# Optimization experiments

Hardware: AMD Instinct MI355X
Metric: run time of the kernel (lower is better)

Reference implementation:

```python
import jax, jax.numpy as jnp
import numpy as np

H = 128            # hidden_channels
HM = 2 * H         # _inner_mlp_mult * H
N = 50000          # num nodes
E = 400000         # num edges
M = 800000         # num node-edge incidences (2 per edge)
BN_EPS = 1e-5


def _bn_relu(x, g, b):
    # BatchNorm1d in training mode: population stats over the batch dim, then affine + ReLU
    m = x.mean(0)
    v = ((x - m) ** 2).mean(0)
    return jax.nn.relu((x - m) * jax.lax.rsqrt(v + BN_EPS) * g + b)


def setup_inputs() -> dict:
    key = jax.random.key(0)
    ks = jax.random.split(key, 12)
    node_rep = jax.random.normal(ks[0], (N, H), dtype=jnp.float32)
    edge_rep = jax.random.normal(ks[1], (E, H), dtype=jnp.float32)
    src = jax.random.randint(ks[2], (M,), 0, N, dtype=jnp.int32)
    dst = jax.random.randint(ks[3], (M,), 0, E, dtype=jnp.int32)
    node2edge_index = jnp.stack([src, dst], 0)

    def lin(k, fan_in, fan_out):
        return jax.random.normal(k, (fan_in, fan_out), dtype=jnp.float32) / np.sqrt(fan_in)

    return {
        "node_rep": node_rep,
        "edge_rep": edge_rep,
        "node2edge_index": node2edge_index,
        # lvl_mlp_1: Linear(2H->H, no bias), BN(H), ReLU
        "Wa": lin(ks[4], 2 * H, H), "ga": jnp.ones((H,)), "ba": jnp.zeros((H,)),
        # lvl_mlp_2: Linear(H->2H), BN, ReLU, Linear(2H->H), BN, ReLU
        "Wb1": lin(ks[5], H, HM), "gb1": jnp.ones((HM,)), "bb1": jnp.zeros((HM,)),
        "Wb2": lin(ks[6], HM, H), "gb2": jnp.ones((H,)), "bb2": jnp.zeros((H,)),
        # lift_mlp: Linear(H->2H), BN, ReLU, Linear(2H->H), BN, ReLU
        "Wl1": lin(ks[7], H, HM), "gl1": jnp.ones((HM,)), "bl1": jnp.zeros((HM,)),
        "Wl2": lin(ks[8], HM, H), "gl2": jnp.ones((H,)), "bl2": jnp.zeros((H,)),
        "eps1": jnp.zeros(()), "eps2": jnp.zeros(()),
    }


def reference(node_rep, edge_rep, node2edge_index,
              Wa, ga, ba,
              Wb1, gb1, bb1, Wb2, gb2, bb2,
              Wl1, gl1, bl1, Wl2, gl2, bl2,
              eps1, eps2):
    src = node2edge_index[0]  # node index per incidence
    dst = node2edge_index[1]  # edge index per incidence

    # node -> edge gather + scatter_sum
    node2edge_val = node_rep[src]                                   # [M, H]
    lift_aggr = jax.ops.segment_sum(node2edge_val, dst, num_segments=E)  # [E, H]

    # lvl_mlp_1 on concatenated edge features
    lvl_aggr_edge = _bn_relu(jnp.concatenate([lift_aggr, edge_rep], -1) @ Wa, ga, ba)  # [E, H]

    # edge -> node gather + scatter_sum
    lvl_aggr = jax.ops.segment_sum(lvl_aggr_edge[dst], src, num_segments=N)  # [N, H]

    # lvl_mlp_2
    hn = (1.0 + eps1) * node_rep + lvl_aggr
    node_out = _bn_relu(_bn_relu(hn @ Wb1, gb1, bb1) @ Wb2, gb2, bb2)

    # lift_mlp
    he = (1.0 + eps2) * edge_rep + lift_aggr
    edge_out = _bn_relu(_bn_relu(he @ Wl1, gl1, bl1) @ Wl2, gl2, bl2)

    return node_out, edge_out
```

## Files before the change

### kernel.cpp

```cpp
#include <hip/hip_runtime.h>
#include <cstdint>
#include <cstddef>


typedef __bf16 bf16_t;
typedef __bf16 bf16x2 __attribute__((ext_vector_type(2)));
typedef __bf16 bf16x8 __attribute__((ext_vector_type(8)));
typedef float f32x4 __attribute__((ext_vector_type(4)));

__device__ __forceinline__ void atomAddF(float* p, float v) {
  unsafeAtomicAdd(p, v);
}


__global__ __launch_bounds__(256) void k_hist(
    const int* __restrict__ src, const int* __restrict__ dst, int M,
    int* __restrict__ cnt_e, int* __restrict__ cnt_n) {
  int i = blockIdx.x * blockDim.x + threadIdx.x;
  if (i >= M) return;
  atomicAdd(cnt_e + dst[i], 1);
  atomicAdd(cnt_n + src[i], 1);
}

__global__ __launch_bounds__(256) void k_scan_block(
    const int* __restrict__ in, int* __restrict__ out, int* __restrict__ bsum,
    int L) {
  __shared__ int sh[256];
  int t = threadIdx.x;
  int base = (blockIdx.x * 256 + t) * 4;
  int v[4];
#pragma unroll
  for (int j = 0; j < 4; ++j) v[j] = (base + j < L) ? in[base + j] : 0;
  int tsum = v[0] + v[1] + v[2] + v[3];
  sh[t] = tsum;
  __syncthreads();
#pragma unroll
  for (int off = 1; off < 256; off <<= 1) {
    int x = (t >= off) ? sh[t - off] : 0;
    __syncthreads();
    sh[t] += x;
    __syncthreads();
  }
  int excl = sh[t] - tsum;
  if (t == 255) bsum[blockIdx.x] = sh[255];
  int run = excl;
#pragma unroll
  for (int j = 0; j < 4; ++j) {
    if (base + j < L) out[base + j] = run;
    run += v[j];
  }
}

__global__ __launch_bounds__(1024) void k_scan_top(int* __restrict__ bsum,
                                                   int nb) {
  __shared__ int sh[1024];
  __shared__ int running;
  int t = threadIdx.x;
  if (t == 0) running = 0;
  __syncthreads();
  for (int c = 0; c < nb; c += 1024) {
    int i = c + t;
    int v = (i < nb) ? bsum[i] : 0;
    sh[t] = v;
    __syncthreads();
#pragma unroll
    for (int off = 1; off < 1024; off <<= 1) {
      int x = (t >= off) ? sh[t - off] : 0;
      __syncthreads();
      sh[t] += x;
      __syncthreads();
    }
    int r = running;
    if (i < nb) bsum[i] = r + sh[t] - v;
    __syncthreads();
    if (t == 1023) running = r + sh[1023];
    __syncthreads();
  }
}

__global__ __launch_bounds__(256) void k_scan_add(int* __restrict__ out,
                                                  const int* __restrict__ bsum,
                                                  int L) {
  int base = (blockIdx.x * 256 + threadIdx.x) * 4;
  int add = bsum[blockIdx.x];
#pragma unroll
  for (int j = 0; j < 4; ++j)
    if (base + j < L) out[base + j] += add;
}

__global__ void k_settail(int* off_e, int E, int* off_n, int N, int M) {
  off_e[E] = M;
  off_n[N] = M;
}

__global__ __launch_bounds__(256) void k_fill(
    const int* __restrict__ src, const int* __restrict__ dst, int M,
    const int* __restrict__ off_e, int* __restrict__ fill_e,
    int* __restrict__ csr_e, const int* __restrict__ off_n,
    int* __restrict__ fill_n, int* __restrict__ csr_n) {
  int i = blockIdx.x * blockDim.x + threadIdx.x;
  if (i >= M) return;
  int s = src[i], d = dst[i];
  int pe = off_e[d] + atomicAdd(fill_e + d, 1);
  csr_e[pe] = s;
  int pn = off_n[s] + atomicAdd(fill_n + s, 1);
  csr_n[pn] = d;
}

__global__ __launch_bounds__(256) void k_wconv(const float* __restrict__ W,
                                               bf16_t* __restrict__ Wt, int K,
                                               int NC) {
  int idx = blockIdx.x * blockDim.x + threadIdx.x;
  if (idx >= K * NC) return;
  int k = idx / NC, n = idx % NC;
  Wt[(size_t)n * K + k] = (bf16_t)W[idx];
}


__global__ __launch_bounds__(256) void k_gather1(
    const float* __restrict__ node, const float* __restrict__ edge,
    const int* __restrict__ off_e, const int* __restrict__ csr_e,
    const float* __restrict__ eps2p, bf16_t* __restrict__ Xcat,
    bf16_t* __restrict__ he, int E) {
  int e = blockIdx.x * 4 + (threadIdx.x >> 6);
  if (e >= E) return;
  int lane = threadIdx.x & 63;
  float a2 = 1.0f + eps2p[0];
  int b = off_e[e], en = off_e[e + 1];
  float2 acc = make_float2(0.f, 0.f);
  const float2* np = (const float2*)node;
  for (int j = b; j < en; ++j) {
    int r = csr_e[j];
    float2 v = np[(size_t)r * 64 + lane];
    acc.x += v.x;
    acc.y += v.y;
  }
  float2 ev = ((const float2*)edge)[(size_t)e * 64 + lane];
  bf16x2* xr = (bf16x2*)(Xcat + (size_t)e * 256);
  bf16x2 lb; lb[0] = (bf16_t)acc.x; lb[1] = (bf16_t)acc.y;
  bf16x2 eb; eb[0] = (bf16_t)ev.x; eb[1] = (bf16_t)ev.y;
  xr[lane] = lb;
  xr[lane + 64] = eb;
  bf16x2 hb;
  hb[0] = (bf16_t)fmaf(a2, ev.x, acc.x);
  hb[1] = (bf16_t)fmaf(a2, ev.y, acc.y);
  ((bf16x2*)(he + (size_t)e * 128))[lane] = hb;
}

__global__ __launch_bounds__(256) void k_gather2(
    const bf16_t* __restrict__ Y1, const float* __restrict__ st,
    const float* __restrict__ node, const int* __restrict__ off_n,
    const int* __restrict__ csr_n, const float* __restrict__ eps1p,
    bf16_t* __restrict__ hn, int N) {
  int n = blockIdx.x * 4 + (threadIdx.x >> 6);
  if (n >= N) return;
  int lane = threadIdx.x & 63;
  float a1 = 1.0f + eps1p[0];
  float2 sc = ((const float2*)st)[lane];
  float2 tc = ((const float2*)(st + 128))[lane];
  int b = off_n[n], en = off_n[n + 1];
  float2 acc = make_float2(0.f, 0.f);
  for (int j = b; j < en; ++j) {
    int r = csr_n[j];
    bf16x2 y = ((const bf16x2*)(Y1 + (size_t)r * 128))[lane];
    acc.x += fmaxf(fmaf((float)y[0], sc.x, tc.x), 0.f);
    acc.y += fmaxf(fmaf((float)y[1], sc.y, tc.y), 0.f);
  }
  float2 nv = ((const float2*)node)[(size_t)n * 64 + lane];
  bf16x2 hb;
  hb[0] = (bf16_t)fmaf(a1, nv.x, acc.x);
  hb[1] = (bf16_t)fmaf(a1, nv.y, acc.y);
  ((bf16x2*)(hn + (size_t)n * 128))[lane] = hb;
}


__global__ void k_bnfin(const float* __restrict__ sums, int C, int R,
                        const float* __restrict__ g, const float* __restrict__ b,
                        float* __restrict__ st) {
  int c = blockIdx.x * blockDim.x + threadIdx.x;
  if (c >= C) return;
  float invR = 1.f / (float)R;
  float mean = sums[c] * invR;
  float var = fmaxf(sums[C + c] * invR - mean * mean, 0.f);
  float s = g[c] * rsqrtf(var + 1e-5f);
  st[c] = s;
  st[C + c] = fmaf(-mean, s, b[c]);
}

__global__ __launch_bounds__(256) void k_bnrelu_out(
    const bf16_t* __restrict__ Y, const float* __restrict__ st, long R,
    float* __restrict__ out) {
  long t = (long)blockIdx.x * blockDim.x + threadIdx.x;
  long idx = t * 8;
  if (idx >= R * 128) return;
  int c = (int)(idx & 127);
  bf16x8 y = *(const bf16x8*)(Y + idx);
  float4 s0 = *(const float4*)(st + c);
  float4 s1 = *(const float4*)(st + c + 4);
  float4 t0 = *(const float4*)(st + 128 + c);
  float4 t1 = *(const float4*)(st + 128 + c + 4);
  float4 o0, o1;
  o0.x = fmaxf(fmaf((float)y[0], s0.x, t0.x), 0.f);
  o0.y = fmaxf(fmaf((float)y[1], s0.y, t0.y), 0.f);
  o0.z = fmaxf(fmaf((float)y[2], s0.z, t0.z), 0.f);
  o0.w = fmaxf(fmaf((float)y[3], s0.w, t0.w), 0.f);
  o1.x = fmaxf(fmaf((float)y[4], s1.x, t1.x), 0.f);
  o1.y = fmaxf(fmaf((float)y[5], s1.y, t1.y), 0.f);
  o1.z = fmaxf(fmaf((float)y[6], s1.z, t1.z), 0.f);
  o1.w = fmaxf(fmaf((float)y[7], s1.w, t1.w), 0.f);
  *(float4*)(out + idx) = o0;
  *(float4*)(out + idx + 4) = o1;
}

#define LDSTR 40

template <int TRANSFORM>
__global__ __launch_bounds__(256) void k_mfma_gemm(
    const bf16_t* __restrict__ A, const bf16_t* __restrict__ Wt,
    const float* __restrict__ st, float* __restrict__ gstats,
    bf16_t* __restrict__ Y, int R, int K, int NCtot) {
  __shared__ bf16_t As[128 * LDSTR];
  __shared__ bf16_t Bs[128 * LDSTR];
  const int tid = threadIdx.x;
  const int wave = tid >> 6;
  const int lane = tid & 63;
  const int quad = lane >> 4;
  const int l16 = lane & 15;
  const int wm = wave & 1;
  const int wn = wave >> 1;
  const int r0 = blockIdx.x * 128;
  const int n0 = blockIdx.y * 128;

  f32x4 acc[4][4] = {};

  const int srow = tid >> 2;
  const int sk = (tid & 3) * 8;

  for (int k0 = 0; k0 < K; k0 += 32) {
#pragma unroll
    for (int p = 0; p < 2; ++p) {
      int row = p * 64 + srow;
      int gr = r0 + row;
      if (gr >= R) gr = R - 1;
      bf16x8 v = *(const bf16x8*)(A + (size_t)gr * K + k0 + sk);
      if (TRANSFORM) {
        bf16x8 o;
#pragma unroll
        for (int i = 0; i < 8; ++i) {
          float f = (float)v[i];
          float s = st[k0 + sk + i];
          float b = st[K + k0 + sk + i];
          o[i] = (bf16_t)fmaxf(fmaf(f, s, b), 0.f);
        }
        v = o;
      }
      *(bf16x8*)&As[row * LDSTR + sk] = v;
    }
#pragma unroll
    for (int p = 0; p < 2; ++p) {
      int row = p * 64 + srow;
      bf16x8 v = *(const bf16x8*)(Wt + (size_t)(n0 + row) * K + k0 + sk);
      *(bf16x8*)&Bs[row * LDSTR + sk] = v;
    }
    __syncthreads();
    bf16x8 af[4], bfr[4];
#pragma unroll
    for (int i = 0; i < 4; ++i)
      af[i] = *(const bf16x8*)&As[(wm * 64 + i * 16 + l16) * LDSTR + quad * 8];
#pragma unroll
    for (int j = 0; j < 4; ++j)
      bfr[j] = *(const bf16x8*)&Bs[(wn * 64 + j * 16 + l16) * LDSTR + quad * 8];
#pragma unroll
    for (int i = 0; i < 4; ++i)
#pragma unroll
      for (int j = 0; j < 4; ++j)
        acc[i][j] = __builtin_amdgcn_mfma_f32_16x16x32_bf16(af[i], bfr[j],
                                                            acc[i][j], 0, 0, 0);
    __syncthreads();
  }

  float csum[4] = {0.f, 0.f, 0.f, 0.f};
  float csq[4] = {0.f, 0.f, 0.f, 0.f};
#pragma unroll
  for (int i = 0; i < 4; ++i) {
    int baseRow = r0 + wm * 64 + i * 16 + quad * 4;
#pragma unroll
    for (int reg = 0; reg < 4; ++reg) {
      int row = baseRow + reg;
      if (row < R) {
#pragma unroll
        for (int j = 0; j < 4; ++j) {
          float v = acc[i][j][reg];
          int col = n0 + wn * 64 + j * 16 + l16;
          Y[(size_t)row * NCtot + col] = (bf16_t)v;
          csum[j] += v;
          csq[j] += v * v;
        }
      }
    }
  }
  __syncthreads();
  float* Ssum = (float*)As;
  float* Ssq = (float*)As + 1024;
  int contrib = wm * 4 + quad;
#pragma unroll
  for (int j = 0; j < 4; ++j) {
    int c = wn * 64 + j * 16 + l16;
    Ssum[c * 8 + contrib] = csum[j];
    Ssq[c * 8 + contrib] = csq[j];
  }
  __syncthreads();
  if (tid < 128) {
    float s = 0.f;
#pragma unroll
    for (int k = 0; k < 8; ++k) s += Ssum[tid * 8 + k];
    atomAddF(gstats + n0 + tid, s);
  } else {
    int c = tid - 128;
    float q = 0.f;
#pragma unroll
    for (int k = 0; k < 8; ++k) q += Ssq[c * 8 + k];
    atomAddF(gstats + NCtot + n0 + c, q);
  }
}


extern "C" void kernel_launch(void* const* d_in, const int* in_sizes, int n_in,
                              void* d_out, int out_size, void* d_ws,
                              size_t ws_size, hipStream_t stream) {
  const float* node_rep = (const float*)d_in[0];
  const float* edge_rep = (const float*)d_in[1];
  const int* n2e = (const int*)d_in[2];
  const float* Wa = (const float*)d_in[3];
  const float* ga = (const float*)d_in[4];
  const float* ba = (const float*)d_in[5];
  const float* Wb1 = (const float*)d_in[6];
  const float* gb1 = (const float*)d_in[7];
  const float* bb1 = (const float*)d_in[8];
  const float* Wb2 = (const float*)d_in[9];
  const float* gb2 = (const float*)d_in[10];
  const float* bb2 = (const float*)d_in[11];
  const float* Wl1 = (const float*)d_in[12];
  const float* gl1 = (const float*)d_in[13];
  const float* bl1 = (const float*)d_in[14];
  const float* Wl2 = (const float*)d_in[15];
  const float* gl2 = (const float*)d_in[16];
  const float* bl2 = (const float*)d_in[17];
  const float* eps1 = (const float*)d_in[18];
  const float* eps2 = (const float*)d_in[19];

  const int N = in_sizes[0] / 128;
  const int E = in_sizes[1] / 128;
  const int M = in_sizes[2] / 2;
  const int* srcI = n2e;
  const int* dstI = n2e + M;

  char* wsb = (char*)d_ws;
  size_t off = 0;
  auto alloc = [&](size_t bytes) {
    void* p = wsb + off;
    off += (bytes + 255) & ~(size_t)255;
    return p;
  };
  bf16_t* Xcat = (bf16_t*)alloc((size_t)E * 256 * 2);
  bf16_t* he   = (bf16_t*)alloc((size_t)E * 128 * 2);
  bf16_t* Y1   = (bf16_t*)alloc((size_t)E * 128 * 2);
  bf16_t* Ze   = (bf16_t*)alloc((size_t)E * 256 * 2);
  bf16_t* Y2e  = (bf16_t*)alloc((size_t)E * 128 * 2);
  bf16_t* hn   = (bf16_t*)alloc((size_t)N * 128 * 2);
  bf16_t* Zn   = (bf16_t*)alloc((size_t)N * 256 * 2);
  bf16_t* Y2n  = (bf16_t*)alloc((size_t)N * 128 * 2);
  bf16_t* Wa_t  = (bf16_t*)alloc(256 * 128 * 2);
  bf16_t* Wb1_t = (bf16_t*)alloc(128 * 256 * 2);
  bf16_t* Wb2_t = (bf16_t*)alloc(256 * 128 * 2);
  bf16_t* Wl1_t = (bf16_t*)alloc(128 * 256 * 2);
  bf16_t* Wl2_t = (bf16_t*)alloc(256 * 128 * 2);
  int* cnt_e  = (int*)alloc((size_t)E * 4);
  int* off_e  = (int*)alloc((size_t)(E + 1) * 4);
  int* fill_e = (int*)alloc((size_t)E * 4);
  int* csr_e  = (int*)alloc((size_t)M * 4);
  int* cnt_n  = (int*)alloc((size_t)N * 4);
  int* off_n  = (int*)alloc((size_t)(N + 1) * 4);
  int* fill_n = (int*)alloc((size_t)N * 4);
  int* csr_n  = (int*)alloc((size_t)M * 4);
  int* bsumE  = (int*)alloc(4096 * 4);
  int* bsumN  = (int*)alloc(4096 * 4);
  float* stats = (float*)alloc(8192 * 4);

  float* sum_a  = stats + 0;
  float* st_a   = stats + 256;
  float* sum_b1 = stats + 512;
  float* st_b1  = stats + 1024;
  float* sum_b2 = stats + 1536;
  float* st_b2  = stats + 1792;
  float* sum_l1 = stats + 2048;
  float* st_l1  = stats + 2560;
  float* sum_l2 = stats + 3072;
  float* st_l2  = stats + 3328;

  float* node_out = (float*)d_out;
  float* edge_out = (float*)d_out + (size_t)N * 128;

  hipMemsetAsync(stats, 0, 8192 * sizeof(float), stream);
  hipMemsetAsync(cnt_e, 0, (size_t)E * sizeof(int), stream);
  hipMemsetAsync(fill_e, 0, (size_t)E * sizeof(int), stream);
  hipMemsetAsync(cnt_n, 0, (size_t)N * sizeof(int), stream);
  hipMemsetAsync(fill_n, 0, (size_t)N * sizeof(int), stream);

  k_hist<<<(M + 255) / 256, 256, 0, stream>>>(srcI, dstI, M, cnt_e, cnt_n);
  const int nbE = (E + 1023) / 1024;
  const int nbN = (N + 1023) / 1024;
  k_scan_block<<<nbE, 256, 0, stream>>>(cnt_e, off_e, bsumE, E);
  k_scan_top<<<1, 1024, 0, stream>>>(bsumE, nbE);
  k_scan_add<<<nbE, 256, 0, stream>>>(off_e, bsumE, E);
  k_scan_block<<<nbN, 256, 0, stream>>>(cnt_n, off_n, bsumN, N);
  k_scan_top<<<1, 1024, 0, stream>>>(bsumN, nbN);
  k_scan_add<<<nbN, 256, 0, stream>>>(off_n, bsumN, N);
  k_settail<<<1, 1, 0, stream>>>(off_e, E, off_n, N, M);
  k_fill<<<(M + 255) / 256, 256, 0, stream>>>(srcI, dstI, M, off_e, fill_e,
                                              csr_e, off_n, fill_n, csr_n);

  k_wconv<<<128, 256, 0, stream>>>(Wa, Wa_t, 256, 128);
  k_wconv<<<128, 256, 0, stream>>>(Wb1, Wb1_t, 128, 256);
  k_wconv<<<128, 256, 0, stream>>>(Wb2, Wb2_t, 256, 128);
  k_wconv<<<128, 256, 0, stream>>>(Wl1, Wl1_t, 128, 256);
  k_wconv<<<128, 256, 0, stream>>>(Wl2, Wl2_t, 256, 128);

  k_gather1<<<(E + 3) / 4, 256, 0, stream>>>(node_rep, edge_rep, off_e, csr_e,
                                             eps2, Xcat, he, E);

  k_mfma_gemm<0><<<dim3((E + 127) / 128, 1), 256, 0, stream>>>(
      Xcat, Wa_t, nullptr, sum_a, Y1, E, 256, 128);
  k_bnfin<<<1, 256, 0, stream>>>(sum_a, 128, E, ga, ba, st_a);

  k_gather2<<<(N + 3) / 4, 256, 0, stream>>>(Y1, st_a, node_rep, off_n, csr_n,
                                             eps1, hn, N);

  k_mfma_gemm<0><<<dim3((N + 127) / 128, 2), 256, 0, stream>>>(
      hn, Wb1_t, nullptr, sum_b1, Zn, N, 128, 256);
  k_bnfin<<<1, 256, 0, stream>>>(sum_b1, 256, N, gb1, bb1, st_b1);
  k_mfma_gemm<1><<<dim3((N + 127) / 128, 1), 256, 0, stream>>>(
      Zn, Wb2_t, st_b1, sum_b2, Y2n, N, 256, 128);
  k_bnfin<<<1, 256, 0, stream>>>(sum_b2, 128, N, gb2, bb2, st_b2);
  {
    long total = ((long)N * 128 + 7) / 8;
    k_bnrelu_out<<<(int)((total + 255) / 256), 256, 0, stream>>>(Y2n, st_b2, N,
                                                                 node_out);
  }

  k_mfma_gemm<0><<<dim3((E + 127) / 128, 2), 256, 0, stream>>>(
      he, Wl1_t, nullptr, sum_l1, Ze, E, 128, 256);
  k_bnfin<<<1, 256, 0, stream>>>(sum_l1, 256, E, gl1, bl1, st_l1);
  k_mfma_gemm<1><<<dim3((E + 127) / 128, 1), 256, 0, stream>>>(
      Ze, Wl2_t, st_l1, sum_l2, Y2e, E, 256, 128);
  k_bnfin<<<1, 256, 0, stream>>>(sum_l2, 128, E, gl2, bl2, st_l2);
  {
    long total = ((long)E * 128 + 7) / 8;
    k_bnrelu_out<<<(int)((total + 255) / 256), 256, 0, stream>>>(Y2e, st_l2, E,
                                                                 edge_out);
  }
}
```

Baseline: 1.327 ms.

## Fuse edge-feature concat and he computation into first GEMM; widen gather vectors

```diff
diff --git a/kernel.cpp b/kernel.cpp
--- a/kernel.cpp
+++ b/kernel.cpp
@@ -5,6 +5,7 @@
 
 typedef __bf16 bf16_t;
 typedef __bf16 bf16x2 __attribute__((ext_vector_type(2)));
+typedef __bf16 bf16x4 __attribute__((ext_vector_type(4)));
 typedef __bf16 bf16x8 __attribute__((ext_vector_type(8)));
 typedef float f32x4 __attribute__((ext_vector_type(4)));
 
@@ -116,35 +117,23 @@
   Wt[(size_t)n * K + k] = (bf16_t)W[idx];
 }
 
-
 __global__ __launch_bounds__(256) void k_gather1(
-    const float* __restrict__ node, const float* __restrict__ edge,
-    const int* __restrict__ off_e, const int* __restrict__ csr_e,
-    const float* __restrict__ eps2p, bf16_t* __restrict__ Xcat,
-    bf16_t* __restrict__ he, int E) {
-  int e = blockIdx.x * 4 + (threadIdx.x >> 6);
+    const float* __restrict__ node, const int* __restrict__ off_e,
+    const int* __restrict__ csr_e, bf16_t* __restrict__ lift, int E) {
+  int e = blockIdx.x * 8 + (threadIdx.x >> 5);
   if (e >= E) return;
-  int lane = threadIdx.x & 63;
-  float a2 = 1.0f + eps2p[0];
+  int l = threadIdx.x & 31;
   int b = off_e[e], en = off_e[e + 1];
-  float2 acc = make_float2(0.f, 0.f);
-  const float2* np = (const float2*)node;
+  float4 acc = make_float4(0.f, 0.f, 0.f, 0.f);
   for (int j = b; j < en; ++j) {
     int r = csr_e[j];
-    float2 v = np[(size_t)r * 64 + lane];
-    acc.x += v.x;
-    acc.y += v.y;
-  }
-  float2 ev = ((const float2*)edge)[(size_t)e * 64 + lane];
-  bf16x2* xr = (bf16x2*)(Xcat + (size_t)e * 256);
-  bf16x2 lb; lb[0] = (bf16_t)acc.x; lb[1] = (bf16_t)acc.y;
-  bf16x2 eb; eb[0] = (bf16_t)ev.x; eb[1] = (bf16_t)ev.y;
-  xr[lane] = lb;
-  xr[lane + 64] = eb;
-  bf16x2 hb;
-  hb[0] = (bf16_t)fmaf(a2, ev.x, acc.x);
-  hb[1] = (bf16_t)fmaf(a2, ev.y, acc.y);
-  ((bf16x2*)(he + (size_t)e * 128))[lane] = hb;
+    float4 v = *(const float4*)(node + (size_t)r * 128 + l * 4);
+    acc.x += v.x; acc.y += v.y; acc.z += v.z; acc.w += v.w;
+  }
+  bf16x4 o;
+  o[0] = (bf16_t)acc.x; o[1] = (bf16_t)acc.y;
+  o[2] = (bf16_t)acc.z; o[3] = (bf16_t)acc.w;
+  *(bf16x4*)(lift + (size_t)e * 128 + l * 4) = o;
 }
 
 __global__ __launch_bounds__(256) void k_gather2(
@@ -152,25 +141,40 @@
     const float* __restrict__ node, const int* __restrict__ off_n,
     const int* __restrict__ csr_n, const float* __restrict__ eps1p,
     bf16_t* __restrict__ hn, int N) {
-  int n = blockIdx.x * 4 + (threadIdx.x >> 6);
+  int n = blockIdx.x * 16 + (threadIdx.x >> 4);
   if (n >= N) return;
-  int lane = threadIdx.x & 63;
+  int l = threadIdx.x & 15;
   float a1 = 1.0f + eps1p[0];
-  float2 sc = ((const float2*)st)[lane];
-  float2 tc = ((const float2*)(st + 128))[lane];
+  float4 s0 = *(const float4*)(st + l * 8);
+  float4 s1 = *(const float4*)(st + l * 8 + 4);
+  float4 t0 = *(const float4*)(st + 128 + l * 8);
+  float4 t1 = *(const float4*)(st + 128 + l * 8 + 4);
+  float acc[8] = {0.f, 0.f, 0.f, 0.f, 0.f, 0.f, 0.f, 0.f};
   int b = off_n[n], en = off_n[n + 1];
-  float2 acc = make_float2(0.f, 0.f);
   for (int j = b; j < en; ++j) {
     int r = csr_n[j];
-    bf16x2 y = ((const bf16x2*)(Y1 + (size_t)r * 128))[lane];
-    acc.x += fmaxf(fmaf((float)y[0], sc.x, tc.x), 0.f);
-    acc.y += fmaxf(fmaf((float)y[1], sc.y, tc.y), 0.f);
-  }
-  float2 nv = ((const float2*)node)[(size_t)n * 64 + lane];
-  bf16x2 hb;
-  hb[0] = (bf16_t)fmaf(a1, nv.x, acc.x);
-  hb[1] = (bf16_t)fmaf(a1, nv.y, acc.y);
-  ((bf16x2*)(hn + (size_t)n * 128))[lane] = hb;
+    bf16x8 y = *(const bf16x8*)(Y1 + (size_t)r * 128 + l * 8);
+    acc[0] += fmaxf(fmaf((float)y[0], s0.x, t0.x), 0.f);
+    acc[1] += fmaxf(fmaf((float)y[1], s0.y, t0.y), 0.f);
+    acc[2] += fmaxf(fmaf((float)y[2], s0.z, t0.z), 0.f);
+    acc[3] += fmaxf(fmaf((float)y[3], s0.w, t0.w), 0.f);
+    acc[4] += fmaxf(fmaf((float)y[4], s1.x, t1.x), 0.f);
+    acc[5] += fmaxf(fmaf((float)y[5], s1.y, t1.y), 0.f);
+    acc[6] += fmaxf(fmaf((float)y[6], s1.z, t1.z), 0.f);
+    acc[7] += fmaxf(fmaf((float)y[7], s1.w, t1.w), 0.f);
+  }
+  float4 n0 = *(const float4*)(node + (size_t)n * 128 + l * 8);
+  float4 n1 = *(const float4*)(node + (size_t)n * 128 + l * 8 + 4);
+  bf16x8 hb;
+  hb[0] = (bf16_t)fmaf(a1, n0.x, acc[0]);
+  hb[1] = (bf16_t)fmaf(a1, n0.y, acc[1]);
+  hb[2] = (bf16_t)fmaf(a1, n0.z, acc[2]);
+  hb[3] = (bf16_t)fmaf(a1, n0.w, acc[3]);
+  hb[4] = (bf16_t)fmaf(a1, n1.x, acc[4]);
+  hb[5] = (bf16_t)fmaf(a1, n1.y, acc[5]);
+  hb[6] = (bf16_t)fmaf(a1, n1.z, acc[6]);
+  hb[7] = (bf16_t)fmaf(a1, n1.w, acc[7]);
+  *(bf16x8*)(hn + (size_t)n * 128 + l * 8) = hb;
 }
 
 
@@ -232,7 +236,6 @@
   const int n0 = blockIdx.y * 128;
 
   f32x4 acc[4][4] = {};
-
   const int srow = tid >> 2;
   const int sk = (tid & 3) * 8;
 
@@ -321,6 +324,123 @@
 #pragma unroll
     for (int k = 0; k < 8; ++k) q += Ssq[c * 8 + k];
     atomAddF(gstats + NCtot + n0 + c, q);
+  }
+}
+
+__global__ __launch_bounds__(256) void k_mfma_gemm_cat(
+    const bf16_t* __restrict__ lift, const float* __restrict__ edge,
+    const bf16_t* __restrict__ Wt, const float* __restrict__ eps2p,
+    float* __restrict__ gstats, bf16_t* __restrict__ Y,
+    bf16_t* __restrict__ he, int R) {
+  __shared__ bf16_t As[128 * LDSTR];
+  __shared__ bf16_t Bs[128 * LDSTR];
+  const int tid = threadIdx.x;
+  const int wave = tid >> 6;
+  const int lane = tid & 63;
+  const int quad = lane >> 4;
+  const int l16 = lane & 15;
+  const int wm = wave & 1;
+  const int wn = wave >> 1;
+  const int r0 = blockIdx.x * 128;
+  const float a2 = 1.0f + eps2p[0];
+
+  f32x4 acc[4][4] = {};
+  const int srow = tid >> 2;
+  const int sk = (tid & 3) * 8;
+  bf16x8 lreg[4][2];
+
+  for (int ph = 0; ph < 8; ++ph) {
+    const int k0 = ph * 32;
+#pragma unroll
+    for (int p = 0; p < 2; ++p) {
+      int row = p * 64 + srow;
+      int gr = r0 + row;
+      if (gr >= R) gr = R - 1;
+      bf16x8 v;
+      if (ph < 4) {
+        v = *(const bf16x8*)(lift + (size_t)gr * 128 + k0 + sk);
+        lreg[ph][p] = v;
+      } else {
+        const int kk = k0 - 128;
+        float4 e0 = *(const float4*)(edge + (size_t)gr * 128 + kk + sk);
+        float4 e1 = *(const float4*)(edge + (size_t)gr * 128 + kk + sk + 4);
+        const float ef[8] = {e0.x, e0.y, e0.z, e0.w, e1.x, e1.y, e1.z, e1.w};
+        bf16x8 lv = lreg[ph - 4][p];
+        bf16x8 hv;
+#pragma unroll
+        for (int i = 0; i < 8; ++i) {
+          v[i] = (bf16_t)ef[i];
+          hv[i] = (bf16_t)fmaf(a2, ef[i], (float)lv[i]);
+        }
+        *(bf16x8*)(he + (size_t)gr * 128 + kk + sk) = hv;
+      }
+      *(bf16x8*)&As[row * LDSTR + sk] = v;
+    }
+#pragma unroll
+    for (int p = 0; p < 2; ++p) {
+      int row = p * 64 + srow;
+      bf16x8 v = *(const bf16x8*)(Wt + (size_t)row * 256 + k0 + sk);
+      *(bf16x8*)&Bs[row * LDSTR + sk] = v;
+    }
+    __syncthreads();
+    bf16x8 af[4], bfr[4];
+#pragma unroll
+    for (int i = 0; i < 4; ++i)
+      af[i] = *(const bf16x8*)&As[(wm * 64 + i * 16 + l16) * LDSTR + quad * 8];
+#pragma unroll
+    for (int j = 0; j < 4; ++j)
+      bfr[j] = *(const bf16x8*)&Bs[(wn * 64 + j * 16 + l16) * LDSTR + quad * 8];
+#pragma unroll
+    for (int i = 0; i < 4; ++i)
+#pragma unroll
+      for (int j = 0; j < 4; ++j)
+        acc[i][j] = __builtin_amdgcn_mfma_f32_16x16x32_bf16(af[i], bfr[j],
+                                                            acc[i][j], 0, 0, 0);
+    __syncthreads();
+  }
+
+  float csum[4] = {0.f, 0.f, 0.f, 0.f};
+  float csq[4] = {0.f, 0.f, 0.f, 0.f};
+#pragma unroll
+  for (int i = 0; i < 4; ++i) {
+    int baseRow = r0 + wm * 64 + i * 16 + quad * 4;
+#pragma unroll
+    for (int reg = 0; reg < 4; ++reg) {
+      int row = baseRow + reg;
+      if (row < R) {
+#pragma unroll
+        for (int j = 0; j < 4; ++j) {
+          float v = acc[i][j][reg];
+          int col = wn * 64 + j * 16 + l16;
+          Y[(size_t)row * 128 + col] = (bf16_t)v;
+          csum[j] += v;
+          csq[j] += v * v;
+        }
+      }
+    }
+  }
+  __syncthreads();
+  float* Ssum = (float*)As;
+  float* Ssq = (float*)As + 1024;
+  int contrib = wm * 4 + quad;
+#pragma unroll
+  for (int j = 0; j < 4; ++j) {
+    int c = wn * 64 + j * 16 + l16;
+    Ssum[c * 8 + contrib] = csum[j];
+    Ssq[c * 8 + contrib] = csq[j];
+  }
+  __syncthreads();
+  if (tid < 128) {
+    float s = 0.f;
+#pragma unroll
+    for (int k = 0; k < 8; ++k) s += Ssum[tid * 8 + k];
+    atomAddF(gstats + tid, s);
+  } else {
+    int c = tid - 128;
+    float q = 0.f;
+#pragma unroll
+    for (int k = 0; k < 8; ++k) q += Ssq[c * 8 + k];
+    atomAddF(gstats + 128 + c, q);
   }
 }
 
@@ -362,7 +482,7 @@
     off += (bytes + 255) & ~(size_t)255;
     return p;
   };
-  bf16_t* Xcat = (bf16_t*)alloc((size_t)E * 256 * 2);
+  bf16_t* lift = (bf16_t*)alloc((size_t)E * 128 * 2);
   bf16_t* he   = (bf16_t*)alloc((size_t)E * 128 * 2);
   bf16_t* Y1   = (bf16_t*)alloc((size_t)E * 128 * 2);
   bf16_t* Ze   = (bf16_t*)alloc((size_t)E * 256 * 2);
@@ -375,17 +495,18 @@
   bf16_t* Wb2_t = (bf16_t*)alloc(256 * 128 * 2);
   bf16_t* Wl1_t = (bf16_t*)alloc(128 * 256 * 2);
   bf16_t* Wl2_t = (bf16_t*)alloc(256 * 128 * 2);
-  int* cnt_e  = (int*)alloc((size_t)E * 4);
+  int* zbase  = (int*)alloc(((size_t)E * 2 + (size_t)N * 2 + 8192) * 4);
+  int* cnt_e  = zbase;
+  int* fill_e = zbase + E;
+  int* cnt_n  = zbase + 2 * (size_t)E;
+  int* fill_n = zbase + 2 * (size_t)E + N;
+  float* stats = (float*)(zbase + 2 * (size_t)E + 2 * (size_t)N);
   int* off_e  = (int*)alloc((size_t)(E + 1) * 4);
-  int* fill_e = (int*)alloc((size_t)E * 4);
   int* csr_e  = (int*)alloc((size_t)M * 4);
-  int* cnt_n  = (int*)alloc((size_t)N * 4);
   int* off_n  = (int*)alloc((size_t)(N + 1) * 4);
-  int* fill_n = (int*)alloc((size_t)N * 4);
   int* csr_n  = (int*)alloc((size_t)M * 4);
   int* bsumE  = (int*)alloc(4096 * 4);
   int* bsumN  = (int*)alloc(4096 * 4);
-  float* stats = (float*)alloc(8192 * 4);
 
   float* sum_a  = stats + 0;
   float* st_a   = stats + 256;
@@ -401,11 +522,7 @@
   float* node_out = (float*)d_out;
   float* edge_out = (float*)d_out + (size_t)N * 128;
 
-  hipMemsetAsync(stats, 0, 8192 * sizeof(float), stream);
-  hipMemsetAsync(cnt_e, 0, (size_t)E * sizeof(int), stream);
-  hipMemsetAsync(fill_e, 0, (size_t)E * sizeof(int), stream);
-  hipMemsetAsync(cnt_n, 0, (size_t)N * sizeof(int), stream);
-  hipMemsetAsync(fill_n, 0, (size_t)N * sizeof(int), stream);
+  hipMemsetAsync(zbase, 0, ((size_t)E * 2 + (size_t)N * 2 + 8192) * 4, stream);
 
   k_hist<<<(M + 255) / 256, 256, 0, stream>>>(srcI, dstI, M, cnt_e, cnt_n);
   const int nbE = (E + 1023) / 1024;
@@ -426,15 +543,14 @@
   k_wconv<<<128, 256, 0, stream>>>(Wl1, Wl1_t, 128, 256);
   k_wconv<<<128, 256, 0, stream>>>(Wl2, Wl2_t, 256, 128);
 
-  k_gather1<<<(E + 3) / 4, 256, 0, stream>>>(node_rep, edge_rep, off_e, csr_e,
-                                             eps2, Xcat, he, E);
-
-  k_mfma_gemm<0><<<dim3((E + 127) / 128, 1), 256, 0, stream>>>(
-      Xcat, Wa_t, nullptr, sum_a, Y1, E, 256, 128);
+  k_gather1<<<(E + 7) / 8, 256, 0, stream>>>(node_rep, off_e, csr_e, lift, E);
+
+  k_mfma_gemm_cat<<<dim3((E + 127) / 128), 256, 0, stream>>>(
+      lift, edge_rep, Wa_t, eps2, sum_a, Y1, he, E);
   k_bnfin<<<1, 256, 0, stream>>>(sum_a, 128, E, ga, ba, st_a);
 
-  k_gather2<<<(N + 3) / 4, 256, 0, stream>>>(Y1, st_a, node_rep, off_n, csr_n,
-                                             eps1, hn, N);
+  k_gather2<<<(N + 15) / 16, 256, 0, stream>>>(Y1, st_a, node_rep, off_n,
+                                               csr_n, eps1, hn, N);
 
   k_mfma_gemm<0><<<dim3((N + 127) / 128, 2), 256, 0, stream>>>(
       hn, Wb1_t, nullptr, sum_b1, Zn, N, 128, 256);
```

Result: faster. 1.202 ms (-9.4%).
